# Kernel tuning notes

Hardware: AMD Instinct MI355X
Metric: run time of the kernel (lower is better)

Reference implementation:

```python
import jax, jax.numpy as jnp
import numpy as np

B = 8192
N_COLS = 64
D = 1024
EPS = 1e-5


def _layernorm(x, g, b):
    m = jnp.mean(x, axis=-1, keepdims=True)
    v = jnp.mean(jnp.square(x - m), axis=-1, keepdims=True)
    return (x - m) * jax.lax.rsqrt(v + EPS) * g + b


def setup_inputs() -> dict:
    key = jax.random.key(0)
    ks = jax.random.split(key, 8)
    s = 0.02
    return {
        "x1_enc": jax.random.normal(ks[0], (1, N_COLS, D), jnp.float32),
        "x2_enc": jax.random.normal(ks[1], (B, D), jnp.float32),
        "We": jax.random.normal(ks[2], (4, 2 * D, D), jnp.float32) * s,
        "be": jnp.zeros((4, D), jnp.float32),
        "W1": jax.random.normal(ks[3], (2 * D, 4 * D), jnp.float32) * s,
        "b1": jnp.zeros((4 * D,), jnp.float32),
        "g1": jnp.ones((4 * D,), jnp.float32),
        "bt1": jnp.zeros((4 * D,), jnp.float32),
        "W2": jax.random.normal(ks[4], (4 * D, 2 * D), jnp.float32) * s,
        "b2": jnp.zeros((2 * D,), jnp.float32),
        "g2": jnp.ones((2 * D,), jnp.float32),
        "bt2": jnp.zeros((2 * D,), jnp.float32),
        "W3": jax.random.normal(ks[5], (2 * D, 1), jnp.float32) * s,
        "b3": jnp.zeros((1,), jnp.float32),
        "col_pairs": jax.random.randint(ks[6], (B, 2), 0, N_COLS, jnp.int64),
        "vis_type": jax.random.randint(ks[7], (B,), 0, 4, jnp.int64),
    }


def reference(x1_enc, x2_enc, We, be, W1, b1, g1, bt1, W2, b2, g2, bt2, W3, b3,
              col_pairs, vis_type):
    # x1 repeated B times is identical per row -> gather directly from x1_enc[0]
    x11 = x1_enc[0, col_pairs[:, 0]]          # [B, D]
    x12 = x1_enc[0, col_pairs[:, 1]]          # [B, D]
    x1c = jnp.concatenate([x11, x12], axis=1)  # [B, 2D]

    # 1-of-4 expert routing: compute all experts, select by vis_type
    all_y = jax.nn.relu(jnp.einsum('bd,edk->bek', x1c, We) + be)  # [B, 4, D]
    y1 = jnp.take_along_axis(all_y, vis_type[:, None, None], axis=1)[:, 0]  # [B, D]

    y = jnp.concatenate([y1, x2_enc], axis=1)  # [B, 2D]
    h = _layernorm(jax.nn.relu(y @ W1 + b1), g1, bt1)
    h = _layernorm(jax.nn.relu(h @ W2 + b2), g2, bt2)
    return jax.nn.sigmoid(h @ W3 + b3)  # [B, 1]
```

## Files before the change

kernel.cpp:

```cpp
#include <hip/hip_runtime.h>

typedef unsigned short u16;
typedef __bf16 bf16x8 __attribute__((ext_vector_type(8)));
typedef float f32x4v __attribute__((ext_vector_type(4)));
typedef u16 u16x8 __attribute__((ext_vector_type(8)));

__device__ __forceinline__ u16 f2bf(float f) {
  union { float f; unsigned u; } v; v.f = f;
  unsigned r = v.u + 0x7fffu + ((v.u >> 16) & 1u);
  return (u16)(r >> 16);
}
__device__ __forceinline__ float bf2f(u16 h) {
  union { unsigned u; float f; } v; v.u = ((unsigned)h) << 16;
  return v.f;
}

#define G2L16(g, l)                                                            \
  __builtin_amdgcn_global_load_lds((__attribute__((address_space(1))) void*)(g), \
                                   (__attribute__((address_space(3))) void*)(l), 16, 0, 0)

__global__ __launch_bounds__(256) void k_transpose2(const float* __restrict__ W1,
                                                    u16* __restrict__ W1T,
                                                    const float* __restrict__ W2,
                                                    u16* __restrict__ W2gT,
                                                    const float* __restrict__ g1,
                                                    const float* __restrict__ bt1,
                                                    float* __restrict__ w2ps,
                                                    float* __restrict__ w2pc,
                                                    const float* __restrict__ g2,
                                                    const float* __restrict__ bt2,
                                                    const float* __restrict__ W3,
                                                    float* __restrict__ scal) {
  const int t = threadIdx.x;
  int bid = blockIdx.x;
  if (bid == 4096) {
    __shared__ float red[8];
    float sg = 0.f, cb = 0.f;
    for (int i = 0; i < 8; ++i) {
      int c = i * 256 + t;
      float w3 = W3[c];
      sg += g2[c] * w3;
      cb += bt2[c] * w3;
    }
#pragma unroll
    for (int off = 32; off > 0; off >>= 1) {
      sg += __shfl_down(sg, off, 64);
      cb += __shfl_down(cb, off, 64);
    }
    const int lane = t & 63, wv = t >> 6;
    if (lane == 0) { red[wv] = sg; red[4 + wv] = cb; }
    __syncthreads();
    if (t == 0) {
      scal[0] = red[0] + red[1] + red[2] + red[3];
      scal[1] = red[4] + red[5] + red[6] + red[7];
    }
    return;
  }
  __shared__ float tile[64][65];
  const float* in;
  u16* out;
  int R, C, bx, by, fold;
  if (bid < 2048) {
    in = W1; out = W1T; R = 2048; C = 4096; fold = 0;
    bx = bid & 63; by = bid >> 6;
  } else {
    bid -= 2048;
    in = W2; out = W2gT; R = 4096; C = 2048; fold = 1;
    bx = bid & 31; by = bid >> 5;
  }
  const int c0 = bx * 64, r0 = by * 64;
  const int tc = (t & 15) * 4, tr = t >> 4;
#pragma unroll
  for (int i = 0; i < 4; ++i) {
    int r = tr + i * 16;
    f32x4v v = *(const f32x4v*)(in + (size_t)(r0 + r) * C + c0 + tc);
    tile[r][tc] = v[0]; tile[r][tc + 1] = v[1];
    tile[r][tc + 2] = v[2]; tile[r][tc + 3] = v[3];
  }
  __syncthreads();
  const int oc = t >> 2;
  const int rb = (t & 3) * 16;
  float gv[16];
#pragma unroll
  for (int i = 0; i < 16; ++i) gv[i] = fold ? g1[r0 + rb + i] : 1.f;
  u16x8 o0, o1;
#pragma unroll
  for (int i = 0; i < 8; ++i) o0[i] = f2bf(tile[rb + i][oc] * gv[i]);
#pragma unroll
  for (int i = 0; i < 8; ++i) o1[i] = f2bf(tile[rb + 8 + i][oc] * gv[8 + i]);
  *(u16x8*)(out + (size_t)(c0 + oc) * R + r0 + rb) = o0;
  *(u16x8*)(out + (size_t)(c0 + oc) * R + r0 + rb + 8) = o1;
  if (fold) {
    float ps = 0.f, pc = 0.f;
#pragma unroll
    for (int i = 0; i < 16; ++i) {
      float w = tile[rb + i][oc];
      ps += gv[i] * w;
      pc += bt1[r0 + rb + i] * w;
    }
    ps += __shfl_down(ps, 2, 4); ps += __shfl_down(ps, 1, 4);
    pc += __shfl_down(pc, 2, 4); pc += __shfl_down(pc, 1, 4);
    if ((t & 3) == 0) {
      w2ps[(size_t)(c0 + oc) * 64 + by] = ps;
      w2pc[(size_t)(c0 + oc) * 64 + by] = pc;
    }
  }
}

__global__ __launch_bounds__(256) void k_pq(const float* __restrict__ x1,
                                            const float* __restrict__ We,
                                            float* __restrict__ pq0,
                                            float* __restrict__ pq1) {
  const int n0 = blockIdx.x * 64;
  const int ep = blockIdx.y;
  const int e = ep >> 1, p = ep & 1;
  const int khalf = blockIdx.z & 1;
  const int chalf = blockIdx.z >> 1;
  const int ks = khalf * 512;
  float* pq = khalf ? pq1 : pq0;
  __shared__ float As[32][33];
  __shared__ float Bs[32][68];
  const int t = threadIdx.x;
  const int tx = t & 15, ty = t >> 4;
  float acc[2][4] = {};
  const float* wbase = We + (size_t)e * 2048 * 1024 + (size_t)p * 1024 * 1024;
  for (int k0 = ks; k0 < ks + 512; k0 += 32) {
#pragma unroll
    for (int i = 0; i < 4; ++i) {
      int ix = t + i * 256;
      As[ix >> 5][ix & 31] =
          x1[(size_t)(chalf * 32 + (ix >> 5)) * 1024 + k0 + (ix & 31)];
    }
#pragma unroll
    for (int i = 0; i < 8; ++i) {
      int ix = t + i * 256;
      Bs[ix >> 6][ix & 63] = wbase[(size_t)(k0 + (ix >> 6)) * 1024 + n0 + (ix & 63)];
    }
    __syncthreads();
#pragma unroll
    for (int kk = 0; kk < 32; ++kk) {
      float av[2];
#pragma unroll
      for (int i = 0; i < 2; ++i) av[i] = As[ty * 2 + i][kk];
      f32x4v bv = *(const f32x4v*)&Bs[kk][tx * 4];
#pragma unroll
      for (int i = 0; i < 2; ++i)
#pragma unroll
        for (int j = 0; j < 4; ++j) acc[i][j] += av[i] * bv[j];
    }
    __syncthreads();
  }
#pragma unroll
  for (int i = 0; i < 2; ++i) {
    float* dst = pq + ((size_t)ep * 64 + chalf * 32 + ty * 2 + i) * 1024 + n0 + tx * 4;
#pragma unroll
    for (int j = 0; j < 4; ++j) dst[j] = acc[i][j];
  }
}

__global__ __launch_bounds__(256) void k_build_y(const float* __restrict__ pq0,
                                                 const float* __restrict__ pq1,
                                                 const float* __restrict__ x2,
                                                 const float* __restrict__ be,
                                                 const int* __restrict__ cp,
                                                 const int* __restrict__ vis,
                                                 u16* __restrict__ Y) {
  const int t = threadIdx.x;
  for (int rr = 0; rr < 8; ++rr) {
    const int b = blockIdx.x * 8 + rr;
    const int e = vis[b];
    u16x8 o;
    if (t < 128) {
      const int c0 = cp[2 * b], c1 = cp[2 * b + 1];
      const size_t po = ((size_t)(e * 2) * 64 + c0) * 1024 + t * 8;
      const size_t qo = ((size_t)(e * 2 + 1) * 64 + c1) * 1024 + t * 8;
      const float* B = be + e * 1024 + t * 8;
#pragma unroll
      for (int i = 0; i < 8; ++i) {
        float v = pq0[po + i] + pq1[po + i] + pq0[qo + i] + pq1[qo + i] + B[i];
        o[i] = f2bf(v > 0.f ? v : 0.f);
      }
      *(u16x8*)(Y + (size_t)b * 2048 + t * 8) = o;
    } else {
      const float* X = x2 + (size_t)b * 1024 + (size_t)(t - 128) * 8;
#pragma unroll
      for (int i = 0; i < 8; ++i) o[i] = f2bf(X[i]);
      *(u16x8*)(Y + (size_t)b * 2048 + 1024 + (size_t)(t - 128) * 8) = o;
    }
  }
}

template <int MODE>
__global__ __launch_bounds__(256, 3) void k_gemm(const u16* __restrict__ A,
                                                 const u16* __restrict__ BT,
                                                 const float* __restrict__ bias,
                                                 float2* __restrict__ sp,
                                                 const float* __restrict__ w2ps,
                                                 const float* __restrict__ w2pc,
                                                 const float* __restrict__ b2,
                                                 const float* __restrict__ g2,
                                                 const float* __restrict__ W3,
                                                 float4* __restrict__ part,
                                                 u16* __restrict__ C,
                                                 int M, int N, int K) {
  __shared__ u16 As[128 * 64];
  __shared__ u16 Bs[128 * 64];
  const int tid = threadIdx.x;
  const int lane = tid & 63;
  const int wave = tid >> 6;

  const int nx = gridDim.x, ny = gridDim.y;
  const int bid = blockIdx.y * nx + blockIdx.x;
  const int stripe = ny >> 3;
  const int xcd = bid & 7;
  const int loc = bid >> 3;
  const int panel = loc / (stripe * 4);
  const int rem = loc - panel * (stripe * 4);
  const int by = xcd * stripe + (rem >> 2);
  const int bx = panel * 4 + (rem & 3);
  const int tileN = bx * 128;
  const int tileM = by * 128;
  const int wm = wave & 1;
  const int wn = wave >> 1;

  f32x4v acc[4][4];
#pragma unroll
  for (int i = 0; i < 4; ++i)
#pragma unroll
    for (int j = 0; j < 4; ++j) acc[i][j] = (f32x4v){0.f, 0.f, 0.f, 0.f};

  const int srow = tid >> 3;
  const int lchunk = (tid & 7) ^ (srow & 7);
  const u16* aptr = A + (size_t)(tileM + srow) * K + lchunk * 8;
  const u16* bptr = BT + (size_t)(tileN + srow) * K + lchunk * 8;
  u16* asp = As + tid * 8;
  u16* bsp = Bs + tid * 8;

  const int s = lane & 7;
  const int kp0 = ((lane >> 4) ^ s) * 8;
  const int kp1 = kp0 ^ 32;
  const int am = wm * 64 + (lane & 15);
  const int bn = wn * 64 + (lane & 15);

  for (int k0 = 0; k0 < K; k0 += 64) {
    G2L16(aptr, asp);
    G2L16(aptr + (size_t)32 * K, asp + 2048);
    G2L16(aptr + (size_t)64 * K, asp + 4096);
    G2L16(aptr + (size_t)96 * K, asp + 6144);
    G2L16(bptr, bsp);
    G2L16(bptr + (size_t)32 * K, bsp + 2048);
    G2L16(bptr + (size_t)64 * K, bsp + 4096);
    G2L16(bptr + (size_t)96 * K, bsp + 6144);
    aptr += 64;
    bptr += 64;
    __syncthreads();

    bf16x8 af[4], bfr[4];
#pragma unroll
    for (int mi = 0; mi < 4; ++mi)
      af[mi] = *(const bf16x8*)(As + (am + mi * 16) * 64 + kp0);
#pragma unroll
    for (int ni = 0; ni < 4; ++ni)
      bfr[ni] = *(const bf16x8*)(Bs + (bn + ni * 16) * 64 + kp0);
#pragma unroll
    for (int mi = 0; mi < 4; ++mi)
#pragma unroll
      for (int ni = 0; ni < 4; ++ni)
        acc[mi][ni] = __builtin_amdgcn_mfma_f32_16x16x32_bf16(af[mi], bfr[ni], acc[mi][ni], 0, 0, 0);
#pragma unroll
    for (int mi = 0; mi < 4; ++mi)
      af[mi] = *(const bf16x8*)(As + (am + mi * 16) * 64 + kp1);
#pragma unroll
    for (int ni = 0; ni < 4; ++ni)
      bfr[ni] = *(const bf16x8*)(Bs + (bn + ni * 16) * 64 + kp1);
#pragma unroll
    for (int mi = 0; mi < 4; ++mi)
#pragma unroll
      for (int ni = 0; ni < 4; ++ni)
        acc[mi][ni] = __builtin_amdgcn_mfma_f32_16x16x32_bf16(af[mi], bfr[ni], acc[mi][ni], 0, 0, 0);
    __syncthreads();
  }

  const int crow = tileM + wm * 64 + (lane >> 4) * 4;
  const int ccol = tileN + wn * 64 + (lane & 15);
  const int cb = bx * 2 + wn;

  if (MODE == 0) {
    float cv0[4];
#pragma unroll
    for (int ni = 0; ni < 4; ++ni) cv0[ni] = bias[ccol + ni * 16];
#pragma unroll
    for (int mi = 0; mi < 4; ++mi) {
#pragma unroll
      for (int r = 0; r < 4; ++r) {
        const int row = crow + mi * 16 + r;
        float s_ = 0.f, ss_ = 0.f;
#pragma unroll
        for (int ni = 0; ni < 4; ++ni) {
          float v = acc[mi][ni][r] + cv0[ni];
          v = v > 0.f ? v : 0.f;
          s_ += v; ss_ += v * v;
          C[(size_t)row * N + ccol + ni * 16] = f2bf(v);
        }
#pragma unroll
        for (int off = 8; off >= 1; off >>= 1) {
          s_ += __shfl_xor(s_, off, 16);
          ss_ += __shfl_xor(ss_, off, 16);
        }
        if ((lane & 15) == 0)
          sp[(size_t)row * 64 + cb] = make_float2(s_, ss_);
      }
    }
  } else {
    __shared__ float2 stL[128];
    __shared__ float s1L[128];
    __shared__ float c1bL[128];
    {
      const int rr = tid >> 1, hf = tid & 1;
      float s_ = 0.f, ss_ = 0.f;
      const float2* sprow = sp + (size_t)(tileM + rr) * 64 + hf * 32;
#pragma unroll
      for (int i = 0; i < 32; ++i) { float2 p = sprow[i]; s_ += p.x; ss_ += p.y; }
      s_ += __shfl_xor(s_, 1);
      ss_ += __shfl_xor(ss_, 1);
      if (hf == 0) {
        float m = s_ * (1.f / 4096.f);
        float var = ss_ * (1.f / 4096.f) - m * m;
        stL[rr] = make_float2(m, rsqrtf(var + 1e-5f));
      }
      float a_ = 0.f, b_ = 0.f;
      const float* wp = w2ps + (size_t)(tileN + rr) * 64 + hf * 32;
      const float* wc = w2pc + (size_t)(tileN + rr) * 64 + hf * 32;
#pragma unroll
      for (int i = 0; i < 32; ++i) { a_ += wp[i]; b_ += wc[i]; }
      a_ += __shfl_xor(a_, 1);
      b_ += __shfl_xor(b_, 1);
      if (hf == 0) {
        s1L[rr] = a_;
        c1bL[rr] = b_ + b2[tileN + rr];
      }
    }
    __syncthreads();
    float cv0[4], cv1[4], cg[4];
#pragma unroll
    for (int ni = 0; ni < 4; ++ni) {
      const int c = ccol + ni * 16;
      const int lc = c - tileN;
      cv0[ni] = s1L[lc];
      cv1[ni] = c1bL[lc];
      cg[ni] = g2[c] * W3[c];
    }
#pragma unroll
    for (int mi = 0; mi < 4; ++mi) {
#pragma unroll
      for (int r = 0; r < 4; ++r) {
        const int row = crow + mi * 16 + r;
        float2 st = stL[row - tileM];
        const float m = st.x, rs = st.y;
        float s_ = 0.f, ss_ = 0.f, d_ = 0.f;
#pragma unroll
        for (int ni = 0; ni < 4; ++ni) {
          float v = rs * acc[mi][ni][r] - rs * m * cv0[ni] + cv1[ni];
          v = v > 0.f ? v : 0.f;
          s_ += v; ss_ += v * v; d_ += v * cg[ni];
        }
#pragma unroll
        for (int off = 8; off >= 1; off >>= 1) {
          s_ += __shfl_xor(s_, off, 16);
          ss_ += __shfl_xor(ss_, off, 16);
          d_ += __shfl_xor(d_, off, 16);
        }
        if ((lane & 15) == 0)
          part[(size_t)row * 32 + cb] = make_float4(s_, ss_, d_, 0.f);
      }
    }
  }
}

__global__ __launch_bounds__(256) void k_final(const float4* __restrict__ part,
                                               const float* __restrict__ scal,
                                               const float* __restrict__ b3,
                                               float* __restrict__ out) {
  const int t = threadIdx.x;
  const int g = t >> 4, l = t & 15;
  const int row = blockIdx.x * 16 + g;
  float4 a = part[(size_t)row * 32 + l * 2];
  float4 b = part[(size_t)row * 32 + l * 2 + 1];
  float S = a.x + b.x, SS = a.y + b.y, D = a.z + b.z;
#pragma unroll
  for (int off = 8; off >= 1; off >>= 1) {
    S += __shfl_xor(S, off, 16);
    SS += __shfl_xor(SS, off, 16);
    D += __shfl_xor(D, off, 16);
  }
  if (l == 0) {
    float m = S * (1.f / 2048.f);
    float rs = rsqrtf(SS * (1.f / 2048.f) - m * m + 1e-5f);
    float logit = rs * D - rs * m * scal[0] + scal[1] + b3[0];
    out[row] = 1.f / (1.f + expf(-logit));
  }
}

extern "C" void kernel_launch(void* const* d_in, const int* in_sizes, int n_in,
                              void* d_out, int out_size, void* d_ws, size_t ws_size,
                              hipStream_t stream) {
  const float* x1 = (const float*)d_in[0];
  const float* x2 = (const float*)d_in[1];
  const float* We = (const float*)d_in[2];
  const float* be = (const float*)d_in[3];
  const float* W1 = (const float*)d_in[4];
  const float* b1 = (const float*)d_in[5];
  const float* g1 = (const float*)d_in[6];
  const float* bt1 = (const float*)d_in[7];
  const float* W2 = (const float*)d_in[8];
  const float* b2 = (const float*)d_in[9];
  const float* g2 = (const float*)d_in[10];
  const float* bt2 = (const float*)d_in[11];
  const float* W3 = (const float*)d_in[12];
  const float* b3 = (const float*)d_in[13];
  const int* cp = (const int*)d_in[14];
  const int* vis = (const int*)d_in[15];
  float* out = (float*)d_out;

  char* ws = (char*)d_ws;
  u16* W1T  = (u16*)(ws);
  u16* W2gT = (u16*)(ws + 16777216);
  u16* Y    = (u16*)(ws + 33554432);
  u16* H1   = (u16*)(ws + 67108864);
  float* PQ0 = (float*)(ws + 134217728);
  float* PQ1 = (float*)(ws + 136314880);
  float2* sp = (float2*)(ws + 134217728);
  float4* part = (float4*)(ws + 138412032);
  float* s1u  = (float*)(ws + 142606336);
  float* w2ps = (float*)(ws + 142614528);
  float* w2pc = (float*)(ws + 143138816);
  float* scal = (float*)(ws + 143663104);
  (void)s1u; (void)bt1;

  k_transpose2<<<4097, 256, 0, stream>>>(W1, W1T, W2, W2gT, g1, bt1,
                                         w2ps, w2pc, g2, bt2, W3, scal);
  k_pq<<<dim3(16, 8, 4), 256, 0, stream>>>(x1, We, PQ0, PQ1);
  k_build_y<<<1024, 256, 0, stream>>>(PQ0, PQ1, x2, be, cp, vis, Y);
  k_gemm<0><<<dim3(32, 64), 256, 0, stream>>>(
      Y, W1T, b1, sp, nullptr, nullptr, nullptr, nullptr, nullptr, nullptr,
      H1, 8192, 4096, 2048);
  k_gemm<1><<<dim3(16, 64), 256, 0, stream>>>(
      H1, W2gT, nullptr, sp, w2ps, w2pc, b2, g2, W3, part, nullptr,
      8192, 2048, 4096);
  k_final<<<512, 256, 0, stream>>>(part, scal, b3, out);
}
```

Baseline: 475.8 us.

## Fuse final layernorm-sigmoid reduction into second GEMM via last-block atomic counter

Removes the separate final kernel by having the last column block for each row tile (detected with an atomic counter) reduce the per-row partial statistics and write the sigmoid output. It also raises the GEMM launch-bounds occupancy hint from 3 to 4 blocks per CU. A memset of the counters is added each call. The tighter register budget from the occupancy change may cause spills in the GEMM inner loop.

```diff
diff --git a/kernel.cpp b/kernel.cpp
--- a/kernel.cpp
+++ b/kernel.cpp
@@ -191,7 +191,7 @@
 }
 
 template <int MODE>
-__global__ __launch_bounds__(256, 3) void k_gemm(const u16* __restrict__ A,
+__global__ __launch_bounds__(256, 4) void k_gemm(const u16* __restrict__ A,
                                                  const u16* __restrict__ BT,
                                                  const float* __restrict__ bias,
                                                  float2* __restrict__ sp,
@@ -202,6 +202,10 @@
                                                  const float* __restrict__ W3,
                                                  float4* __restrict__ part,
                                                  u16* __restrict__ C,
+                                                 const float* __restrict__ scal,
+                                                 const float* __restrict__ b3,
+                                                 float* __restrict__ out,
+                                                 int* __restrict__ cnt,
                                                  int M, int N, int K) {
   __shared__ u16 As[128 * 64];
   __shared__ u16 Bs[128 * 64];
@@ -374,30 +378,27 @@
           part[(size_t)row * 32 + cb] = make_float4(s_, ss_, d_, 0.f);
       }
     }
-  }
-}
-
-__global__ __launch_bounds__(256) void k_final(const float4* __restrict__ part,
-                                               const float* __restrict__ scal,
-                                               const float* __restrict__ b3,
-                                               float* __restrict__ out) {
-  const int t = threadIdx.x;
-  const int g = t >> 4, l = t & 15;
-  const int row = blockIdx.x * 16 + g;
-  float4 a = part[(size_t)row * 32 + l * 2];
-  float4 b = part[(size_t)row * 32 + l * 2 + 1];
-  float S = a.x + b.x, SS = a.y + b.y, D = a.z + b.z;
-#pragma unroll
-  for (int off = 8; off >= 1; off >>= 1) {
-    S += __shfl_xor(S, off, 16);
-    SS += __shfl_xor(SS, off, 16);
-    D += __shfl_xor(D, off, 16);
-  }
-  if (l == 0) {
-    float m = S * (1.f / 2048.f);
-    float rs = rsqrtf(SS * (1.f / 2048.f) - m * m + 1e-5f);
-    float logit = rs * D - rs * m * scal[0] + scal[1] + b3[0];
-    out[row] = 1.f / (1.f + expf(-logit));
+    __shared__ int lastv;
+    __threadfence();
+    __syncthreads();
+    if (tid == 0) lastv = atomicAdd(&cnt[by], 1);
+    __syncthreads();
+    if (lastv == 15) {
+      __threadfence();
+      if (tid < 128) {
+        const int row = tileM + tid;
+        float S = 0.f, SS = 0.f, D = 0.f;
+#pragma unroll 4
+        for (int i = 0; i < 32; ++i) {
+          float4 p = part[(size_t)row * 32 + i];
+          S += p.x; SS += p.y; D += p.z;
+        }
+        float m = S * (1.f / 2048.f);
+        float rs = rsqrtf(SS * (1.f / 2048.f) - m * m + 1e-5f);
+        float logit = rs * D - rs * m * scal[0] + scal[1] + b3[0];
+        out[row] = 1.f / (1.f + expf(-logit));
+      }
+    }
   }
 }
 
@@ -431,21 +432,21 @@
   float* PQ1 = (float*)(ws + 136314880);
   float2* sp = (float2*)(ws + 134217728);
   float4* part = (float4*)(ws + 138412032);
-  float* s1u  = (float*)(ws + 142606336);
-  float* w2ps = (float*)(ws + 142614528);
-  float* w2pc = (float*)(ws + 143138816);
-  float* scal = (float*)(ws + 143663104);
-  (void)s1u; (void)bt1;
-
+  float* w2ps = (float*)(ws + 142606336);
+  float* w2pc = (float*)(ws + 143130624);
+  float* scal = (float*)(ws + 143654912);
+  int* cnt    = (int*)(ws + 143654920);
+  (void)bt1;
+
+  hipMemsetAsync(cnt, 0, 64 * sizeof(int), stream);
   k_transpose2<<<4097, 256, 0, stream>>>(W1, W1T, W2, W2gT, g1, bt1,
                                          w2ps, w2pc, g2, bt2, W3, scal);
   k_pq<<<dim3(16, 8, 4), 256, 0, stream>>>(x1, We, PQ0, PQ1);
   k_build_y<<<1024, 256, 0, stream>>>(PQ0, PQ1, x2, be, cp, vis, Y);
   k_gemm<0><<<dim3(32, 64), 256, 0, stream>>>(
       Y, W1T, b1, sp, nullptr, nullptr, nullptr, nullptr, nullptr, nullptr,
-      H1, 8192, 4096, 2048);
+      H1, nullptr, nullptr, nullptr, nullptr, 8192, 4096, 2048);
   k_gemm<1><<<dim3(16, 64), 256, 0, stream>>>(
       H1, W2gT, nullptr, sp, w2ps, w2pc, b2, g2, W3, part, nullptr,
-      8192, 2048, 4096);
-  k_final<<<512, 256, 0, stream>>>(part, scal, b3, out);
-}
+      scal, b3, out, cnt, 8192, 2048, 4096);
+}
```

New measurement: 583.8 us. 22.7% more time.
